# Optimization experiments

Hardware: AMD Instinct MI355X
Metric: run time of the kernel (lower is better)

The kernel has to match this reference:

```python
import jax, jax.numpy as jnp
import numpy as np

NUM_E = 20000   # entities
NUM_R = 200     # relations (rel table has 2*NUM_R rows)
H = 200         # h_dim
TD = 48         # t_dim (UnionTimeEncode: two halves of 24)
HD = TD // 2
L_HIST = 32     # padded per-(batch,k) history list length
HIS_K = 3
N_HIST = 3      # len(his_list_g)
N_LAYERS = 2    # RGCN layers (config.num_layers)
E = 200000      # edges per historical graph
BATCH = 512


def setup_inputs() -> dict:
    key = jax.random.key(0)
    ks = jax.random.split(key, 32)
    nrm = lambda k, shape, s=0.05: (jax.random.normal(k, shape, jnp.float32) * s)
    inp = {}
    # graph / index inputs (int)
    inp['src'] = jax.random.randint(ks[0], (N_HIST, E), 0, NUM_E, jnp.int32)
    inp['dst'] = jax.random.randint(ks[1], (N_HIST, E), 0, NUM_E, jnp.int32)
    inp['etype'] = jax.random.randint(ks[2], (N_HIST, E), 0, 2 * NUM_R, jnp.int32)
    inp['data'] = jax.random.randint(ks[3], (BATCH, 4), 0, NUM_R, jnp.int32)  # s,r,o,t
    inp['his_idx'] = jax.random.randint(ks[4], (BATCH, HIS_K, L_HIST), 0, NUM_E, jnp.int32)
    inp['his_len'] = jax.random.randint(ks[5], (BATCH, HIS_K), 0, L_HIST + 1, jnp.int32)
    # parameters (float)
    inp['ent'] = nrm(ks[6], (NUM_E, H), 0.5)          # EntEmb.ent (normal init)
    inp['loop_weight'] = nrm(ks[7], (H, H))           # EntEmb self-loop weight
    inp['rel'] = nrm(ks[8], (2 * NUM_R, H), 0.5)
    # UnionTimeEncode params (AbsTimeEncode v=0 + CosTimeEncode)
    basis = (1.0 / 10 ** np.linspace(0.0, 9.0, HD)).astype(np.float32)
    inp['abs_freq'] = jnp.asarray(basis)
    inp['abs_phase'] = jnp.zeros((HD,), jnp.float32)
    inp['cos_freq'] = jnp.asarray(basis)
    inp['cos_phase'] = jnp.zeros((HD,), jnp.float32)
    # RGCN (RE-GCN style Union-RGCN layer: msg=(h_src+rel_e)@Wn, mean agg, self-loop)
    inp['Wn'] = nrm(ks[9], (N_LAYERS, H, H))
    inp['Ws'] = nrm(ks[10], (N_LAYERS, H, H))
    # GRUCell (PyTorch layout)
    inp['W_ih'] = nrm(ks[11], (3 * H, H + TD))
    inp['W_hh'] = nrm(ks[12], (3 * H, H))
    inp['b_ih'] = jnp.zeros((3 * H,), jnp.float32)
    inp['b_hh'] = jnp.zeros((3 * H,), jnp.float32)
    # attention fusion
    inp['Wb_w'] = nrm(ks[13], (H, 3 * H + TD))
    inp['Wb_b'] = jnp.zeros((H,), jnp.float32)
    inp['Wc_w'] = nrm(ks[14], (1, H))
    inp['Wc_b'] = jnp.zeros((1,), jnp.float32)
    # decoder (MLP query @ entity table)
    inp['Wd_w'] = nrm(ks[15], (H, 3 * H))
    inp['Wd_b'] = jnp.zeros((H,), jnp.float32)
    return inp


def _l2n(x, eps=1e-12):
    # F.normalize: x / max(||x||, eps)
    n = jnp.linalg.norm(x, axis=-1, keepdims=True)
    return x / jnp.maximum(n, eps)


def reference(src, dst, etype, data, his_idx, his_len,
              ent, loop_weight, rel, abs_freq, abs_phase, cos_freq, cos_phase,
              Wn, Ws, W_ih, W_hh, b_ih, b_hh, Wb_w, Wb_b, Wc_w, Wc_b, Wd_w, Wd_b):
    def tenc(t):  # t: [N,1] float -> [N,TD]
        a = jnp.tanh((t + 1.0) * abs_freq + abs_phase)   # AbsTimeEncode(act=tanh)
        c = jnp.cos(t * cos_freq + cos_phase)            # CosTimeEncode
        return jnp.concatenate([a, c], axis=1)

    s_i, r_i = data[:, 0], data[:, 1]
    ent_e = ent @ loop_weight                  # EntEmb self-loop (dropout=identity, eval)
    rel_n = _l2n(rel)
    prev = _l2n(ent_e)                         # g_list[0]
    tim_cnt = N_HIST
    ones_e = jnp.ones((E,), jnp.float32)
    for i in range(N_HIST):                    # python loop over fixed #graphs
        si, di, ei = src[i], dst[i], etype[i]
        deg = jax.ops.segment_sum(ones_e, di, num_segments=NUM_E)         # in-degree
        inv = 1.0 / jnp.maximum(deg, 1.0)
        # g.update_all(copy_src, mean): zero in-degree nodes -> 0
        agg = jax.ops.segment_sum(prev[si], di, num_segments=NUM_E) * inv[:, None]
        h = _l2n(jnp.where(deg[:, None] > 0, agg, 0.0))
        tim_cnt -= 1
        tim = jnp.where(deg > 0, float(tim_cnt), 100.0)[:, None]
        te = tenc(tim)                                                     # [NUM_E,TD]
        for l in range(N_LAYERS):              # RGCN
            msg = (h[si] + rel_n[ei]) @ Wn[l]                              # [E,H]
            nagg = jax.ops.segment_sum(msg, di, num_segments=NUM_E) * inv[:, None]
            h = jax.nn.relu(nagg + h @ Ws[l])
        h = _l2n(h)
        # GRUCell(cat([h, te]), prev)
        gi = jnp.concatenate([h, te], axis=1) @ W_ih.T + b_ih
        gh = prev @ W_hh.T + b_hh
        ir, iz, iN = jnp.split(gi, 3, axis=1)
        hr, hz, hN = jnp.split(gh, 3, axis=1)
        rg = jax.nn.sigmoid(ir + hr)
        zg = jax.nn.sigmoid(iz + hz)
        ng = jnp.tanh(iN + rg * hN)
        prev = _l2n((1.0 - zg) * ng + zg * prev)
    out = prev

    q_s, q_r = out[s_i], rel_n[r_i]
    tim_cnt = min(N_HIST, HIS_K)
    s_embs, atts = [], []
    pos = jnp.arange(L_HIST)[None, :]
    for k in range(min(N_HIST, HIS_K)):
        tim_cnt -= 1
        ln = his_len[:, k]
        mask = (pos < ln[:, None]).astype(jnp.float32)                     # [B,L]
        # sparse one-hot mm + divide by length
        tmp = jnp.einsum('blh,bl->bh', out[his_idx[:, k, :]], mask)
        tmp = _l2n(tmp / jnp.maximum(ln, 1).astype(jnp.float32)[:, None])
        tim = jnp.where(ln > 0, float(tim_cnt), 100.0)[:, None]
        te = tenc(tim)                                                     # [B,TD]
        s_embs.append(tmp)
        a = jax.nn.relu(jnp.concatenate([q_s, q_r, tmp, te], 1) @ Wb_w.T + Wb_b)
        atts.append(a @ Wc_w.T + Wc_b)                                     # [B,1]
    att = jax.nn.softmax(jnp.stack(atts, axis=1), axis=1)                  # [B,K,1]
    out2 = jnp.sum(jnp.stack(s_embs, axis=1) * att, axis=1)                # bmm fusion
    # decoder: MLP query scored against all entity states
    q = jax.nn.relu(jnp.concatenate([q_s, q_r, out2], 1) @ Wd_w.T + Wd_b)
    return q @ out.T                                                       # [B,NUM_E]
```

## Files before the change

kernel.cpp:

```cpp
#include <hip/hip_runtime.h>
#include <hip/hip_bf16.h>

#define NUM_E   20000
#define H_DIM   200
#define TD_DIM  48
#define HD_DIM  24
#define L_HIST  32
#define N_HIST  3
#define E_EDGES 200000
#define BATCH   512


__device__ inline float wave_sum64(float x) {
    #pragma unroll
    for (int m = 1; m < 64; m <<= 1) x += __shfl_xor(x, m);
    return x;
}

__device__ inline ushort f2bf(float f) {
    unsigned u = __float_as_uint(f);
    u += 0x7fffu + ((u >> 16) & 1u);
    return (ushort)(u >> 16);
}
__device__ inline float bf2f(ushort u) {
    return __uint_as_float(((unsigned)u) << 16);
}
__device__ inline float4 bf4_to_f4(ushort4 v) {
    return (float4){bf2f(v.x), bf2f(v.y), bf2f(v.z), bf2f(v.w)};
}

__global__ void fill_i32(int* __restrict__ p, long n, int v) {
    long i = (long)blockIdx.x * blockDim.x + threadIdx.x;
    if (i < n) p[i] = v;
}

__global__ void bias_sum(float* __restrict__ bsum, const float* __restrict__ b_ih,
                         const float* __restrict__ b_hh) {
    int j = blockIdx.x * 256 + threadIdx.x;
    if (j < 600) bsum[j] = b_ih[j] + b_hh[j];
}

__global__ void cvt_bf16_k(ushort* __restrict__ o, const float* __restrict__ in, long n) {
    long i = (long)blockIdx.x * 256 + threadIdx.x;
    if (i < n) o[i] = f2bf(in[i]);
}

__global__ void make_lo(ushort* __restrict__ lo, const float* __restrict__ x,
                        const ushort* __restrict__ hi, long n) {
    long i = (long)blockIdx.x * 256 + threadIdx.x;
    if (i < n) lo[i] = f2bf(x[i] - bf2f(hi[i]));
}

__global__ void tcvt_bf16_k(ushort* __restrict__ o, const float* __restrict__ in, int R, int C) {
    int i = blockIdx.x * 256 + threadIdx.x;
    if (i >= R * C) return;
    int r = i / C, c = i - r * C;
    o[(size_t)c * R + r] = f2bf(in[i]);
}

struct Segs {
    const float* A[4];
    const float* B[4];
    int lda[4], ldb[4], Ks[4];
    int nseg, Ktot;
};

__device__ inline void seg_find(const Segs& sg, int gk, int& s, int& loc) {
    s = 0; loc = gk;
    #pragma unroll
    for (int t = 0; t < 3; t++) {
        if (s + 1 < sg.nseg && loc >= sg.Ks[s]) { loc -= sg.Ks[s]; s++; }
    }
}

__global__ __launch_bounds__(256) void sgemm_splitk(
    float* __restrict__ P, const Segs sg, int M, int N, int nbx, int nby,
    int KS, int tpc)
{
    __shared__ float As[32][68];
    __shared__ float Bs[32][68];

    int tot = nbx * nby;
    int tot_all = tot * KS;
    int chunk = (tot_all + 7) >> 3;
    int v = (int)(blockIdx.x & 7) * chunk + (int)(blockIdx.x >> 3);
    if (v >= tot_all) return;
    int kc = v / tot;
    int tile = v - kc * tot;
    int by = tile / nbx, bx = tile - by * nbx;
    const int bn = bx * 64;
    const int bm = by * 64;
    const int tid = threadIdx.x;
    const int m0 = (tid >> 4) * 4;
    const int n0 = (tid & 15) * 4;

    float acc[4][4];
    #pragma unroll
    for (int i = 0; i < 4; i++)
        #pragma unroll
        for (int j = 0; j < 4; j++) acc[i][j] = 0.f;

    const int Ktot = sg.Ktot;
    const int ntile = (Ktot + 31) / 32;
    const int kt0 = kc * tpc;
    const int kt1 = min(ntile, kt0 + tpc);

    const int a_m  = tid & 31;
    const int a_k4 = (tid >> 5) * 4;
    const int b1_n = tid & 63;
    const int b1_k = (tid >> 6) * 4;

    float4 ra[2], rb[2];
    auto loadA = [&](int k0) {
        int gk = k0 + a_k4;
        bool kin = gk < Ktot;
        int s = 0, loc = 0;
        if (kin) seg_find(sg, gk, s, loc);
        const float* Ab = sg.A[s];
        const int lda = sg.lda[s];
        #pragma unroll
        for (int r = 0; r < 2; r++) {
            int row = bm + a_m + 32 * r;
            float4 vv = {0.f, 0.f, 0.f, 0.f};
            if (kin && row < M) vv = *(const float4*)(Ab + (size_t)row * lda + loc);
            ra[r] = vv;
        }
    };
    auto loadB = [&](int k0) {
        #pragma unroll
        for (int r = 0; r < 2; r++) {
            int k4 = b1_k + 16 * r;
            int gk = k0 + k4;
            bool kin = gk < Ktot;
            int s = 0, loc = 0;
            if (kin) seg_find(sg, gk, s, loc);
            const float* Bb = sg.B[s];
            const int ldb = sg.ldb[s];
            int gn = bn + b1_n;
            float4 vv = {0.f, 0.f, 0.f, 0.f};
            if (kin && gn < N) vv = *(const float4*)(Bb + (size_t)gn * ldb + loc);
            rb[r] = vv;
        }
    };

    if (kt0 < kt1) {
        loadA(kt0 * 32); loadB(kt0 * 32);
        for (int t = kt0; t < kt1; t++) {
            #pragma unroll
            for (int r = 0; r < 2; r++) {
                int m = a_m + 32 * r;
                As[a_k4 + 0][m] = ra[r].x;
                As[a_k4 + 1][m] = ra[r].y;
                As[a_k4 + 2][m] = ra[r].z;
                As[a_k4 + 3][m] = ra[r].w;
            }
            #pragma unroll
            for (int r = 0; r < 2; r++) {
                int k4 = b1_k + 16 * r;
                Bs[k4 + 0][b1_n] = rb[r].x;
                Bs[k4 + 1][b1_n] = rb[r].y;
                Bs[k4 + 2][b1_n] = rb[r].z;
                Bs[k4 + 3][b1_n] = rb[r].w;
            }
            __syncthreads();
            if (t + 1 < kt1) { loadA((t + 1) * 32); loadB((t + 1) * 32); }
            #pragma unroll 8
            for (int kk = 0; kk < 32; kk++) {
                float4 b = *(float4*)&Bs[kk][n0];
                float4 av = *(float4*)&As[kk][m0];
                float a[4] = {av.x, av.y, av.z, av.w};
                #pragma unroll
                for (int i = 0; i < 4; i++) {
                    acc[i][0] += a[i] * b.x;
                    acc[i][1] += a[i] * b.y;
                    acc[i][2] += a[i] * b.z;
                    acc[i][3] += a[i] * b.w;
                }
            }
            __syncthreads();
        }
    }

    int col = bn + n0;
    if (col < N) {
        #pragma unroll
        for (int i = 0; i < 4; i++) {
            int row = bm + m0 + i;
            if (row < M) {
                float4 o = {acc[i][0], acc[i][1], acc[i][2], acc[i][3]};
                *(float4*)(P + ((size_t)kc * M + row) * N + col) = o;
            }
        }
    }
}

__global__ void reduce_relu(float* __restrict__ out, const float* __restrict__ P,
                            const float* __restrict__ bias, int MN, int N, int KS)
{
    int i = blockIdx.x * 256 + threadIdx.x;
    if (i >= MN) return;
    float s = bias[i % N];
    for (int k = 0; k < KS; k++) s += P[(size_t)k * MN + i];
    out[i] = fmaxf(s, 0.f);
}

__global__ void reduce_relu_split(ushort* __restrict__ qhi, ushort* __restrict__ qlo,
                                  const float* __restrict__ P, const float* __restrict__ bias,
                                  int MN, int N, int KS)
{
    int i = blockIdx.x * 256 + threadIdx.x;
    if (i >= MN) return;
    float s = bias[i % N];
    for (int k = 0; k < KS; k++) s += P[(size_t)k * MN + i];
    s = fmaxf(s, 0.f);
    ushort h = f2bf(s);
    qhi[i] = h;
    qlo[i] = f2bf(s - bf2f(h));
}

typedef __attribute__((ext_vector_type(8))) short bfrag;
typedef __attribute__((ext_vector_type(4))) float ffrag;

struct BfSegs {
    const ushort* A[3];
    const ushort* B[3];
    int lda[3], ldb[3], Ks[3];
    int nseg, Ktot;
};

__device__ inline void bseg_find(const BfSegs& sg, int gk, int& s, int& loc) {
    s = 0; loc = gk;
    #pragma unroll
    for (int t = 0; t < 2; t++) {
        if (s + 1 < sg.nseg && loc >= sg.Ks[s]) { loc -= sg.Ks[s]; s++; }
    }
}

struct GemmDesc {
    BfSegs sg;
    float* C;
    ushort* Cb;
    const float* bias;
    int M, N, ldc;
    int act, flags, order;
    int nbx, nby, blk0, nblk;
};

struct MultiArgs {
    GemmDesc d[3];
    int nd;
    int tot;
};

template<int DI>
__device__ __forceinline__ void gemm_body(const MultiArgs& ma, int v,
                                          ushort* __restrict__ Als,
                                          ushort* __restrict__ Bls)
{
    const GemmDesc& D = ma.d[DI];
    const BfSegs& sg = D.sg;
    const int tile = v - D.blk0;
    int by, bx;
    if (D.order == 0) { by = tile / D.nbx; bx = tile - by * D.nbx; }
    else              { bx = tile / D.nby; by = tile - bx * D.nby; }
    const int bm = by * 64, bn = bx * 64;
    const int M = D.M, N = D.N;

    const int tid  = threadIdx.x;
    const int lane = tid & 63;
    const int w    = tid >> 6;
    const int wm   = (w & 1) * 2;
    const int wn   = (w >> 1) * 2;

    ffrag acc[2][2];
    #pragma unroll
    for (int i = 0; i < 2; i++)
        #pragma unroll
        for (int j = 0; j < 2; j++) acc[i][j] = (ffrag){0.f, 0.f, 0.f, 0.f};

    const int Ktot = sg.Ktot;
    const int nkt = (Ktot + 63) >> 6;

    int a_m[2], a_kq[2], a_wc[2];
    #pragma unroll
    for (int i = 0; i < 2; i++) {
        int c = i * 256 + tid;
        a_m[i] = c & 63; a_kq[i] = c >> 6;
        a_wc[i] = ((a_m[i] >> 4) * 2 + (a_kq[i] >> 2)) * 64 + (a_kq[i] & 3) * 16 + (a_m[i] & 15);
    }
    int b_n[2], b_kq[2], b_wc[2];
    #pragma unroll
    for (int i = 0; i < 2; i++) {
        int c = i * 256 + tid;
        b_n[i] = c & 63; b_kq[i] = c >> 6;
        b_wc[i] = ((b_n[i] >> 4) * 2 + (b_kq[i] >> 2)) * 64 + (b_kq[i] & 3) * 16 + (b_n[i] & 15);
    }

    uint4 ra[2], rb[2];
    auto loadA = [&](int k0) {
        #pragma unroll
        for (int i = 0; i < 2; i++) {
            int gk = k0 + a_kq[i] * 8;
            int row = bm + a_m[i];
            uint4 vv = {0u, 0u, 0u, 0u};
            if (gk < Ktot && row < M) {
                int s, loc; bseg_find(sg, gk, s, loc);
                vv = *(const uint4*)(sg.A[s] + (size_t)row * sg.lda[s] + loc);
            }
            ra[i] = vv;
        }
    };
    auto loadB = [&](int k0) {
        #pragma unroll
        for (int i = 0; i < 2; i++) {
            int gk = k0 + b_kq[i] * 8;
            int gn = bn + b_n[i];
            uint4 vv = {0u, 0u, 0u, 0u};
            if (gk < Ktot && gn < N) {
                int s, loc; bseg_find(sg, gk, s, loc);
                vv = *(const uint4*)(sg.B[s] + (size_t)gn * sg.ldb[s] + loc);
            }
            rb[i] = vv;
        }
    };

    loadA(0); loadB(0);

    for (int t = 0; t < nkt; t++) {
        #pragma unroll
        for (int i = 0; i < 2; i++) *(uint4*)(&Als[a_wc[i] * 8]) = ra[i];
        #pragma unroll
        for (int i = 0; i < 2; i++) *(uint4*)(&Bls[b_wc[i] * 8]) = rb[i];
        __syncthreads();

        if (t + 1 < nkt) { loadA((t + 1) << 6); loadB((t + 1) << 6); }

        #pragma unroll
        for (int kt = 0; kt < 2; kt++) {
            bfrag af[2], bf[2];
            #pragma unroll
            for (int i = 0; i < 2; i++)
                af[i] = *(const bfrag*)(&Als[(((wm + i) * 2 + kt) * 64 + lane) * 8]);
            #pragma unroll
            for (int j = 0; j < 2; j++)
                bf[j] = *(const bfrag*)(&Bls[(((wn + j) * 2 + kt) * 64 + lane) * 8]);
            #pragma unroll
            for (int i = 0; i < 2; i++)
                #pragma unroll
                for (int j = 0; j < 2; j++)
                    acc[i][j] = __builtin_amdgcn_mfma_f32_16x16x32_bf16(af[i], bf[j], acc[i][j], 0, 0, 0);
        }
        __syncthreads();
    }

    const int rbase = (lane >> 4) * 4;
    const int cl = lane & 15;
    #pragma unroll
    for (int j = 0; j < 2; j++) {
        int col = bn + (wn + j) * 16 + cl;
        if (col >= N) continue;
        float bv = D.bias ? D.bias[col] : 0.f;
        #pragma unroll
        for (int i = 0; i < 2; i++) {
            int mrow = bm + (wm + i) * 16 + rbase;
            #pragma unroll
            for (int r = 0; r < 4; r++) {
                int row = mrow + r;
                if (row < M) {
                    float o = acc[i][j][r] + bv;
                    if (D.act == 1) o = fmaxf(o, 0.f);
                    else if (D.act == 2) o = 1.f / (1.f + expf(-o));
                    if (D.flags & 1) D.C[(size_t)row * D.ldc + col] = o;
                    if (D.flags & 2) D.Cb[(size_t)row * D.ldc + col] = f2bf(o);
                }
            }
        }
    }
}

__global__ __launch_bounds__(256) void mfma_multi(MultiArgs ma)
{
    __shared__ __align__(16) ushort Als[4096];
    __shared__ __align__(16) ushort Bls[4096];

    int tot = ma.tot;
    int chunk = (tot + 7) >> 3;
    int v = (int)(blockIdx.x & 7) * chunk + (int)(blockIdx.x >> 3);
    if (v >= tot) return;

    int di = 0;
    if (ma.nd > 1 && v >= ma.d[1].blk0) di = 1;
    if (ma.nd > 2 && v >= ma.d[2].blk0) di = 2;

    if (di == 0)      gemm_body<0>(ma, v, Als, Bls);
    else if (di == 1) gemm_body<1>(ma, v, Als, Bls);
    else              gemm_body<2>(ma, v, Als, Bls);
}


__global__ void count_dst(const int* __restrict__ di, int* __restrict__ cnt, int E) {
    int e = blockIdx.x * 256 + threadIdx.x;
    if (e < E) atomicAdd(&cnt[di[e]], 1);
}

__global__ __launch_bounds__(1024) void scan_rows(
    const int* __restrict__ cnt, int* __restrict__ row_start, int* __restrict__ cursor,
    float* __restrict__ degf, float* __restrict__ invd)
{
    __shared__ int part[1024];
    const int CH = (NUM_E + 1023) / 1024;
    int t = threadIdx.x;
    int base = t * CH;
    int local[32];
    int s = 0;
    for (int j = 0; j < CH; j++) {
        int idx = base + j;
        int c = (idx < NUM_E) ? cnt[idx] : 0;
        local[j] = s; s += c;
    }
    part[t] = s;
    __syncthreads();
    for (int off = 1; off < 1024; off <<= 1) {
        int vv = (t >= off) ? part[t - off] : 0;
        __syncthreads();
        part[t] += vv;
        __syncthreads();
    }
    int pre = (t == 0) ? 0 : part[t - 1];
    for (int j = 0; j < CH; j++) {
        int idx = base + j;
        if (idx < NUM_E) {
            int rs = pre + local[j];
            row_start[idx] = rs;
            cursor[idx] = rs;
            int c = cnt[idx];
            degf[idx] = (float)c;
            invd[idx] = 1.f / fmaxf((float)c, 1.f);
        }
    }
    if (t == 1023) row_start[NUM_E] = part[1023];
}

__global__ void build_perm(const int* __restrict__ si, const int* __restrict__ di,
                           const int* __restrict__ ei, int* __restrict__ cursor,
                           int* __restrict__ ssrc, int* __restrict__ setype, int E)
{
    int e = blockIdx.x * 256 + threadIdx.x;
    if (e >= E) return;
    int pos = atomicAdd(&cursor[di[e]], 1);
    ssrc[pos]   = si[e];
    setype[pos] = ei[e];
}


__global__ __launch_bounds__(256) void seg_gather_norm_bf(
    ushort* __restrict__ bh, const ushort* __restrict__ bprev,
    const int* __restrict__ ssrc, const int* __restrict__ row_start,
    const float* __restrict__ invd)
{
    int v = blockIdx.x * 4 + (threadIdx.x >> 6);
    int lane = threadIdx.x & 63;
    if (v >= NUM_E) return;
    int s0 = row_start[v], s1 = row_start[v + 1];
    bool act = lane < 50;
    float4 acc = {0.f, 0.f, 0.f, 0.f};
    int j = s0;
    for (; j + 1 < s1; j += 2) {
        int sa = ssrc[j], sb = ssrc[j + 1];
        if (act) {
            float4 xa = bf4_to_f4(*(const ushort4*)(bprev + (long)sa * H_DIM + lane * 4));
            float4 xb = bf4_to_f4(*(const ushort4*)(bprev + (long)sb * H_DIM + lane * 4));
            acc.x += xa.x + xb.x; acc.y += xa.y + xb.y;
            acc.z += xa.z + xb.z; acc.w += xa.w + xb.w;
        }
    }
    if (j < s1) {
        int sa = ssrc[j];
        if (act) {
            float4 xa = bf4_to_f4(*(const ushort4*)(bprev + (long)sa * H_DIM + lane * 4));
            acc.x += xa.x; acc.y += xa.y; acc.z += xa.z; acc.w += xa.w;
        }
    }
    float iv = invd[v];
    acc.x *= iv; acc.y *= iv; acc.z *= iv; acc.w *= iv;
    float ss = act ? (acc.x*acc.x + acc.y*acc.y + acc.z*acc.z + acc.w*acc.w) : 0.f;
    ss = wave_sum64(ss);
    float r = 1.f / fmaxf(sqrtf(ss), 1e-12f);
    if (act) {
        ushort4 ob = {f2bf(acc.x * r), f2bf(acc.y * r), f2bf(acc.z * r), f2bf(acc.w * r)};
        *(ushort4*)(bh + (long)v * H_DIM + lane * 4) = ob;
    }
}

__global__ __launch_bounds__(256) void seg_gather_layer_bf(
    ushort* __restrict__ btmp, const ushort* __restrict__ bh, const ushort* __restrict__ brel,
    const int* __restrict__ ssrc, const int* __restrict__ setype,
    const int* __restrict__ row_start, const float* __restrict__ invd)
{
    int v = blockIdx.x * 4 + (threadIdx.x >> 6);
    int lane = threadIdx.x & 63;
    if (v >= NUM_E) return;
    int s0 = row_start[v], s1 = row_start[v + 1];
    bool act = lane < 50;
    float4 acc = {0.f, 0.f, 0.f, 0.f};
    for (int j = s0; j < s1; j++) {
        int s = ssrc[j];
        int t = setype[j];
        if (act) {
            float4 x = bf4_to_f4(*(const ushort4*)(bh   + (long)s * H_DIM + lane * 4));
            float4 y = bf4_to_f4(*(const ushort4*)(brel + (long)t * H_DIM + lane * 4));
            acc.x += x.x + y.x; acc.y += x.y + y.y;
            acc.z += x.z + y.z; acc.w += x.w + y.w;
        }
    }
    float iv = invd[v];
    if (act) {
        ushort4 ob = {f2bf(acc.x * iv), f2bf(acc.y * iv), f2bf(acc.z * iv), f2bf(acc.w * iv)};
        *(ushort4*)(btmp + (long)v * H_DIM + lane * 4) = ob;
    }
}


__global__ __launch_bounds__(256) void l2norm_rows4(
    float* __restrict__ out, ushort* __restrict__ bout,
    const float* __restrict__ in, int nrows)
{
    int v = blockIdx.x * 4 + (threadIdx.x >> 6);
    int lane = threadIdx.x & 63;
    if (v >= nrows) return;
    bool act = lane < 50;
    float4 x = {0.f, 0.f, 0.f, 0.f};
    if (act) x = *(const float4*)(in + (long)v * H_DIM + lane * 4);
    float ss = x.x*x.x + x.y*x.y + x.z*x.z + x.w*x.w;
    ss = wave_sum64(ss);
    float r = 1.f / fmaxf(sqrtf(ss), 1e-12f);
    if (act) {
        long base = (long)v * H_DIM + lane * 4;
        float4 o = {x.x * r, x.y * r, x.z * r, x.w * r};
        *(float4*)(out + base) = o;
        if (bout) {
            ushort4 ob = {f2bf(o.x), f2bf(o.y), f2bf(o.z), f2bf(o.w)};
            *(ushort4*)(bout + base) = ob;
        }
    }
}

__global__ __launch_bounds__(256) void l2norm_bf4(ushort* __restrict__ b, int nrows)
{
    int v = blockIdx.x * 4 + (threadIdx.x >> 6);
    int lane = threadIdx.x & 63;
    if (v >= nrows) return;
    bool act = lane < 50;
    float4 x = {0.f, 0.f, 0.f, 0.f};
    long base = (long)v * H_DIM + lane * 4;
    if (act) x = bf4_to_f4(*(const ushort4*)(b + base));
    float ss = x.x*x.x + x.y*x.y + x.z*x.z + x.w*x.w;
    ss = wave_sum64(ss);
    float r = 1.f / fmaxf(sqrtf(ss), 1e-12f);
    if (act) {
        ushort4 ob = {f2bf(x.x * r), f2bf(x.y * r), f2bf(x.z * r), f2bf(x.w * r)};
        *(ushort4*)(b + base) = ob;
    }
}

__global__ void tenc_ent(ushort* __restrict__ bte, const float* __restrict__ deg,
                         const float* __restrict__ af, const float* __restrict__ ap,
                         const float* __restrict__ cf, const float* __restrict__ cp,
                         float tcnt, int M)
{
    int idx = blockIdx.x * 256 + threadIdx.x;
    if (idx >= M * TD_DIM) return;
    int v = idx / TD_DIM, j = idx % TD_DIM;
    float t = (deg[v] > 0.f) ? tcnt : 100.0f;
    float val;
    if (j < HD_DIM) val = tanhf((t + 1.f) * af[j] + ap[j]);
    else            val = cosf(t * cf[j - HD_DIM] + cp[j - HD_DIM]);
    bte[idx] = f2bf(val);
}

__global__ __launch_bounds__(256) void gru_fused(
    float* __restrict__ prev, ushort* __restrict__ bprev, const float* __restrict__ rz,
    const float* __restrict__ iN, const float* __restrict__ hN)
{
    int v = blockIdx.x * 4 + (threadIdx.x >> 6);
    int lane = threadIdx.x & 63;
    if (v >= NUM_E) return;
    bool act = lane < 50;
    long b200 = (long)v * H_DIM + lane * 4;
    long b400 = (long)v * 400 + lane * 4;
    float4 o = {0.f, 0.f, 0.f, 0.f};
    if (act) {
        float4 r4 = *(const float4*)(rz + b400);
        float4 z4 = *(const float4*)(rz + b400 + 200);
        float4 n4 = *(const float4*)(iN + b200);
        float4 g4 = *(const float4*)(hN + b200);
        float4 p4 = *(const float4*)(prev + b200);
        float ngx = tanhf(n4.x + r4.x * g4.x);
        float ngy = tanhf(n4.y + r4.y * g4.y);
        float ngz = tanhf(n4.z + r4.z * g4.z);
        float ngw = tanhf(n4.w + r4.w * g4.w);
        o.x = (1.f - z4.x) * ngx + z4.x * p4.x;
        o.y = (1.f - z4.y) * ngy + z4.y * p4.y;
        o.z = (1.f - z4.z) * ngz + z4.z * p4.z;
        o.w = (1.f - z4.w) * ngw + z4.w * p4.w;
    }
    float ss = o.x*o.x + o.y*o.y + o.z*o.z + o.w*o.w;
    ss = wave_sum64(ss);
    float r = 1.f / fmaxf(sqrtf(ss), 1e-12f);
    if (act) {
        float4 wv = {o.x * r, o.y * r, o.z * r, o.w * r};
        *(float4*)(prev + b200) = wv;
        ushort4 ob = {f2bf(wv.x), f2bf(wv.y), f2bf(wv.z), f2bf(wv.w)};
        *(ushort4*)(bprev + b200) = ob;
    }
}


__global__ void gather_qs_qr3(float* __restrict__ qs3, float* __restrict__ qr3,
                              const float* __restrict__ out, const float* __restrict__ reln,
                              const int* __restrict__ data)
{
    long i = (long)blockIdx.x * 256 + threadIdx.x;
    if (i >= (long)BATCH * H_DIM) return;
    int b = (int)(i / H_DIM), j = (int)(i % H_DIM);
    float vs = out[(long)data[b * 4 + 0] * H_DIM + j];
    float vr = reln[(long)data[b * 4 + 1] * H_DIM + j];
    const long S = (long)BATCH * H_DIM;
    qs3[i] = vs; qs3[i + S] = vs; qs3[i + 2*S] = vs;
    qr3[i] = vr; qr3[i + S] = vr; qr3[i + 2*S] = vr;
}

__global__ __launch_bounds__(64) void semb_kernel(
    float* __restrict__ semb, const float* __restrict__ out,
    const int* __restrict__ his_idx, const int* __restrict__ his_len)
{
    int b = blockIdx.x, k = blockIdx.y;
    int lane = threadIdx.x;
    int ln = his_len[b * 3 + k];
    if (ln > L_HIST) ln = L_HIST;
    float vals[4] = {0.f, 0.f, 0.f, 0.f};
    for (int l = 0; l < ln; l++) {
        int idx = his_idx[((long)b * 3 + k) * L_HIST + l];
        #pragma unroll
        for (int t = 0; t < 4; t++) {
            int j = lane + t * 64;
            if (j < H_DIM) vals[t] += out[(long)idx * H_DIM + j];
        }
    }
    float scale = 1.f / fmaxf((float)ln, 1.f);
    float ss = 0.f;
    #pragma unroll
    for (int t = 0; t < 4; t++) { vals[t] *= scale; ss += vals[t] * vals[t]; }
    ss = wave_sum64(ss);
    float r = 1.f / fmaxf(sqrtf(ss), 1e-12f);
    #pragma unroll
    for (int t = 0; t < 4; t++) {
        int j = lane + t * 64;
        if (j < H_DIM) semb[((long)k * BATCH + b) * H_DIM + j] = vals[t] * r;
    }
}

__global__ void tenc_batch(float* __restrict__ teb, const int* __restrict__ his_len,
                           const float* __restrict__ af, const float* __restrict__ ap,
                           const float* __restrict__ cf, const float* __restrict__ cp)
{
    int idx = blockIdx.x * 256 + threadIdx.x;
    if (idx >= 3 * BATCH * TD_DIM) return;
    int k = idx / (BATCH * TD_DIM);
    int rem = idx - k * (BATCH * TD_DIM);
    int b = rem / TD_DIM, j = rem % TD_DIM;
    int ln = his_len[b * 3 + k];
    float t = (ln > 0) ? (float)(2 - k) : 100.0f;
    float val;
    if (j < HD_DIM) val = tanhf((t + 1.f) * af[j] + ap[j]);
    else            val = cosf(t * cf[j - HD_DIM] + cp[j - HD_DIM]);
    teb[idx] = val;
}

__global__ __launch_bounds__(256) void att_logits_rows(
    float* __restrict__ atts, const float* __restrict__ a,
    const float* __restrict__ Wc_w, const float* __restrict__ Wc_b)
{
    int row = blockIdx.x * 4 + (threadIdx.x >> 6);
    int lane = threadIdx.x & 63;
    if (row >= 3 * BATCH) return;
    int k = row >> 9;
    int b = row & 511;
    float s = 0.f;
    for (int j = lane; j < H_DIM; j += 64) s += a[(long)row * H_DIM + j] * Wc_w[j];
    s = wave_sum64(s);
    if (lane == 0) atts[b * 3 + k] = s + Wc_b[0];
}

__global__ void softmax_out2(float* __restrict__ out2, const float* __restrict__ atts,
                             const float* __restrict__ semb)
{
    long i = (long)blockIdx.x * 256 + threadIdx.x;
    if (i >= (long)BATCH * H_DIM) return;
    int b = (int)(i / H_DIM), j = (int)(i % H_DIM);
    float l0 = atts[b * 3 + 0], l1 = atts[b * 3 + 1], l2 = atts[b * 3 + 2];
    float m = fmaxf(l0, fmaxf(l1, l2));
    float e0 = expf(l0 - m), e1 = expf(l1 - m), e2 = expf(l2 - m);
    float s = e0 + e1 + e2;
    float v = (e0 * semb[((long)0 * BATCH + b) * H_DIM + j] +
               e1 * semb[((long)1 * BATCH + b) * H_DIM + j] +
               e2 * semb[((long)2 * BATCH + b) * H_DIM + j]) / s;
    out2[i] = v;
}


extern "C" void kernel_launch(void* const* d_in, const int* in_sizes, int n_in,
                              void* d_out, int out_size, void* d_ws, size_t ws_size,
                              hipStream_t stream)
{
    (void)in_sizes; (void)n_in; (void)out_size; (void)ws_size;

    const int*   src     = (const int*)d_in[0];
    const int*   dst     = (const int*)d_in[1];
    const int*   etype   = (const int*)d_in[2];
    const int*   data    = (const int*)d_in[3];
    const int*   his_idx = (const int*)d_in[4];
    const int*   his_len = (const int*)d_in[5];
    const float* ent     = (const float*)d_in[6];
    const float* loop_w  = (const float*)d_in[7];
    const float* rel     = (const float*)d_in[8];
    const float* af      = (const float*)d_in[9];
    const float* ap      = (const float*)d_in[10];
    const float* cf      = (const float*)d_in[11];
    const float* cp      = (const float*)d_in[12];
    const float* Wn      = (const float*)d_in[13];
    const float* Ws      = (const float*)d_in[14];
    const float* W_ih    = (const float*)d_in[15];
    const float* W_hh    = (const float*)d_in[16];
    const float* b_ih    = (const float*)d_in[17];
    const float* b_hh    = (const float*)d_in[18];
    const float* Wb_w    = (const float*)d_in[19];
    const float* Wb_b    = (const float*)d_in[20];
    const float* Wc_w    = (const float*)d_in[21];
    const float* Wc_b    = (const float*)d_in[22];
    const float* Wd_w    = (const float*)d_in[23];
    const float* Wd_b    = (const float*)d_in[24];
    float* out_p = (float*)d_out;

    float* wp = (float*)d_ws;
    size_t off = 0;
    auto alloc = [&](size_t n) {
        size_t n4 = (n + 3) & ~(size_t)3;
        float* p = wp + off; off += n4; return p;
    };
    const long nE200 = (long)NUM_E * H_DIM;
    float* prev   = alloc(nE200);
    float* h1     = alloc(nE200);
    float* tmp    = alloc(nE200);
    float* rz     = out_p;
    ushort* bh0   = (ushort*)alloc(nE200 / 2);
    ushort* bh1   = (ushort*)alloc(nE200 / 2);
    ushort* btmp  = (ushort*)alloc(nE200 / 2);
    ushort* bprev = (ushort*)alloc(nE200 / 2);
    ushort* plo   = (ushort*)alloc(nE200 / 2);
    ushort* bte   = (ushort*)alloc((size_t)NUM_E * TD_DIM / 2);
    ushort* brel  = (ushort*)alloc(400 * H_DIM / 2);
    ushort* bW_ih = (ushort*)alloc(600 * 248 / 2);
    ushort* bW_hh = (ushort*)alloc(600 * 200 / 2);
    ushort* bWn_t = (ushort*)alloc(2 * 200 * 200 / 2);
    ushort* bWs_t = (ushort*)alloc(2 * 200 * 200 / 2);
    ushort* bLp_t = (ushort*)alloc(200 * 200 / 2);
    ushort* qhi   = (ushort*)alloc(BATCH * H_DIM / 2);
    ushort* qlo   = (ushort*)alloc(BATCH * H_DIM / 2);
    float* degf   = alloc(NUM_E);
    float* invd   = alloc(NUM_E);
    float* reln   = alloc(400 * H_DIM);
    float* bsum   = alloc(1024);
    float* qs3    = alloc(3 * BATCH * H_DIM);
    float* qr3    = alloc(3 * BATCH * H_DIM);
    float* semb   = alloc(3 * BATCH * H_DIM);
    float* teb    = alloc(3 * BATCH * TD_DIM);
    float* abuf   = alloc(3 * BATCH * H_DIM);
    float* atts   = alloc(2048);
    float* out2   = alloc(BATCH * H_DIM);
    int* cnt       = (int*)alloc(NUM_E);
    int* row_start = (int*)alloc(NUM_E + 4);
    int* cursor    = (int*)alloc(NUM_E);
    int* ssrc      = (int*)alloc(E_EDGES);
    int* setype    = (int*)alloc(E_EDGES);

    auto nblk = [](long n) { return (unsigned)((n + 255) / 256); };

    auto bseg1 = [](const ushort* A, int la, const ushort* B, int lb, int K) {
        BfSegs s{}; s.A[0]=A; s.lda[0]=la; s.B[0]=B; s.ldb[0]=lb; s.Ks[0]=K;
        s.nseg=1; s.Ktot=K; return s;
    };
    auto bseg2 = [](const ushort* A0, int la0, const ushort* B0, int lb0, int K0,
                    const ushort* A1, int la1, const ushort* B1, int lb1, int K1) {
        BfSegs s{}; s.A[0]=A0; s.lda[0]=la0; s.B[0]=B0; s.ldb[0]=lb0; s.Ks[0]=K0;
        s.A[1]=A1; s.lda[1]=la1; s.B[1]=B1; s.ldb[1]=lb1; s.Ks[1]=K1;
        s.nseg=2; s.Ktot=K0+K1; return s;
    };
    auto bseg3 = [](const ushort* A0, int la0, const ushort* B0, int lb0, int K0,
                    const ushort* A1, int la1, const ushort* B1, int lb1, int K1,
                    const ushort* A2, int la2, const ushort* B2, int lb2, int K2) {
        BfSegs s{}; s.A[0]=A0; s.lda[0]=la0; s.B[0]=B0; s.ldb[0]=lb0; s.Ks[0]=K0;
        s.A[1]=A1; s.lda[1]=la1; s.B[1]=B1; s.ldb[1]=lb1; s.Ks[1]=K1;
        s.A[2]=A2; s.lda[2]=la2; s.B[2]=B2; s.ldb[2]=lb2; s.Ks[2]=K2;
        s.nseg=3; s.Ktot=K0+K1+K2; return s;
    };

    auto desc = [](const BfSegs& sg, float* C, ushort* Cb, const float* bias,
                   int M, int N, int ldc, int act, int flags, int order) {
        GemmDesc D{}; D.sg=sg; D.C=C; D.Cb=Cb; D.bias=bias;
        D.M=M; D.N=N; D.ldc=ldc; D.act=act; D.flags=flags; D.order=order;
        D.nbx=(N+63)>>6; D.nby=(M+63)>>6; D.nblk=D.nbx*D.nby; D.blk0=0;
        return D;
    };
    auto launch_multi = [&](GemmDesc* ds, int nd) {
        MultiArgs ma{};
        int tot = 0;
        for (int i = 0; i < nd; i++) { ds[i].blk0 = tot; tot += ds[i].nblk; ma.d[i] = ds[i]; }
        ma.nd = nd; ma.tot = tot;
        unsigned grid = (unsigned)(((tot + 7) >> 3) << 3);
        mfma_multi<<<grid, 256, 0, stream>>>(ma);
    };

    auto seg3 = [](const float* A0, int la0, const float* B0, int lb0, int K0,
                   const float* A1, int la1, const float* B1, int lb1, int K1,
                   const float* A2, int la2, const float* B2, int lb2, int K2) {
        Segs s{}; s.A[0]=A0; s.lda[0]=la0; s.B[0]=B0; s.ldb[0]=lb0; s.Ks[0]=K0;
        s.A[1]=A1; s.lda[1]=la1; s.B[1]=B1; s.ldb[1]=lb1; s.Ks[1]=K1;
        s.A[2]=A2; s.lda[2]=la2; s.B[2]=B2; s.ldb[2]=lb2; s.Ks[2]=K2;
        s.nseg=3; s.Ktot=K0+K1+K2; return s;
    };
    auto seg4 = [](const float* A0, int la0, const float* B0, int lb0, int K0,
                   const float* A1, int la1, const float* B1, int lb1, int K1,
                   const float* A2, int la2, const float* B2, int lb2, int K2,
                   const float* A3, int la3, const float* B3, int lb3, int K3) {
        Segs s{}; s.A[0]=A0; s.lda[0]=la0; s.B[0]=B0; s.ldb[0]=lb0; s.Ks[0]=K0;
        s.A[1]=A1; s.lda[1]=la1; s.B[1]=B1; s.ldb[1]=lb1; s.Ks[1]=K1;
        s.A[2]=A2; s.lda[2]=la2; s.B[2]=B2; s.ldb[2]=lb2; s.Ks[2]=K2;
        s.A[3]=A3; s.lda[3]=la3; s.B[3]=B3; s.ldb[3]=lb3; s.Ks[3]=K3;
        s.nseg=4; s.Ktot=K0+K1+K2+K3; return s;
    };
    auto splitk = [&](float* P, const Segs& sg, int M, int N, int KS) {
        int nbx = (N + 63) >> 6;
        int nby = (M + 63) >> 6;
        int ntile = (sg.Ktot + 31) / 32;
        int tpc = (ntile + KS - 1) / KS;
        int tot_all = nbx * nby * KS;
        unsigned grid = (unsigned)(((tot_all + 7) >> 3) << 3);
        sgemm_splitk<<<grid, 256, 0, stream>>>(P, sg, M, N, nbx, nby, KS, tpc);
    };

    const unsigned r4 = (NUM_E + 3) / 4;

    l2norm_rows4<<<100, 256, 0, stream>>>(reln, brel, rel, 400);
    bias_sum<<<3, 256, 0, stream>>>(bsum, b_ih, b_hh);
    cvt_bf16_k<<<nblk(600L*248), 256, 0, stream>>>(bW_ih, W_ih, 600L*248);
    cvt_bf16_k<<<nblk(600L*200), 256, 0, stream>>>(bW_hh, W_hh, 600L*200);
    tcvt_bf16_k<<<nblk(40000), 256, 0, stream>>>(bLp_t, loop_w, 200, 200);
    tcvt_bf16_k<<<nblk(40000), 256, 0, stream>>>(bWn_t,          Wn,          200, 200);
    tcvt_bf16_k<<<nblk(40000), 256, 0, stream>>>(bWn_t + 40000,  Wn + 40000,  200, 200);
    tcvt_bf16_k<<<nblk(40000), 256, 0, stream>>>(bWs_t,          Ws,          200, 200);
    tcvt_bf16_k<<<nblk(40000), 256, 0, stream>>>(bWs_t + 40000,  Ws + 40000,  200, 200);

    cvt_bf16_k<<<nblk(nE200), 256, 0, stream>>>(btmp, ent, nE200);
    {
        GemmDesc d0 = desc(bseg1(btmp, H_DIM, bLp_t, H_DIM, H_DIM),
                           tmp, nullptr, nullptr, NUM_E, H_DIM, H_DIM, 0, 1, 0);
        launch_multi(&d0, 1);
    }
    l2norm_rows4<<<r4, 256, 0, stream>>>(prev, bprev, tmp, NUM_E);

    for (int i = 0; i < N_HIST; i++) {
        const int* si = src   + (long)i * E_EDGES;
        const int* di = dst   + (long)i * E_EDGES;
        const int* ei = etype + (long)i * E_EDGES;
        float tcnt = (float)(N_HIST - 1 - i);

        fill_i32<<<nblk(NUM_E), 256, 0, stream>>>(cnt, NUM_E, 0);
        count_dst<<<nblk(E_EDGES), 256, 0, stream>>>(di, cnt, E_EDGES);
        scan_rows<<<1, 1024, 0, stream>>>(cnt, row_start, cursor, degf, invd);
        build_perm<<<nblk(E_EDGES), 256, 0, stream>>>(si, di, ei, cursor, ssrc, setype, E_EDGES);

        seg_gather_norm_bf<<<r4, 256, 0, stream>>>(bh0, bprev, ssrc, row_start, invd);
        tenc_ent<<<nblk((long)NUM_E * TD_DIM), 256, 0, stream>>>(bte, degf, af, ap, cf, cp, tcnt, NUM_E);

        seg_gather_layer_bf<<<r4, 256, 0, stream>>>(btmp, bh0, brel, ssrc, setype, row_start, invd);
        {
            GemmDesc d0 = desc(bseg2(btmp, H_DIM, bWn_t,         H_DIM, H_DIM,
                                     bh0,  H_DIM, bWs_t,         H_DIM, H_DIM),
                               nullptr, bh1, nullptr, NUM_E, H_DIM, H_DIM, 1, 2, 0);
            launch_multi(&d0, 1);
        }
        seg_gather_layer_bf<<<r4, 256, 0, stream>>>(btmp, bh1, brel, ssrc, setype, row_start, invd);
        {
            GemmDesc d0 = desc(bseg2(btmp, H_DIM, bWn_t + 40000, H_DIM, H_DIM,
                                     bh1,  H_DIM, bWs_t + 40000, H_DIM, H_DIM),
                               nullptr, bh0, nullptr, NUM_E, H_DIM, H_DIM, 1, 2, 0);
            launch_multi(&d0, 1);
        }
        l2norm_bf4<<<r4, 256, 0, stream>>>(bh0, NUM_E);

        {
            GemmDesc d3[3];
            d3[0] = desc(bseg3(bh0,   H_DIM,  bW_ih,       248, H_DIM,
                               bte,   TD_DIM, bW_ih + 200, 248, TD_DIM,
                               bprev, H_DIM,  bW_hh,       200, H_DIM),
                         rz, nullptr, bsum, NUM_E, 400, 400, 2, 1, 0);
            d3[1] = desc(bseg2(bh0, H_DIM,  bW_ih + 400*248,       248, H_DIM,
                               bte, TD_DIM, bW_ih + 400*248 + 200, 248, TD_DIM),
                         h1, nullptr, b_ih + 400, NUM_E, H_DIM, H_DIM, 0, 1, 0);
            d3[2] = desc(bseg1(bprev, H_DIM, bW_hh + 400*200, 200, H_DIM),
                         tmp, nullptr, b_hh + 400, NUM_E, H_DIM, H_DIM, 0, 1, 0);
            launch_multi(d3, 3);
        }

        gru_fused<<<r4, 256, 0, stream>>>(prev, bprev, rz, h1, tmp);
    }

    gather_qs_qr3<<<nblk((long)BATCH * H_DIM), 256, 0, stream>>>(qs3, qr3, prev, reln, data);
    semb_kernel<<<dim3(BATCH, 3), 64, 0, stream>>>(semb, prev, his_idx, his_len);
    tenc_batch<<<nblk(3L * BATCH * TD_DIM), 256, 0, stream>>>(teb, his_len, af, ap, cf, cp);

    {
        const int KS = 8;
        const int MN = 3 * BATCH * H_DIM;
        splitk(h1, seg4(qs3, H_DIM,  Wb_w,       648, H_DIM,
                        qr3, H_DIM,  Wb_w + 200, 648, H_DIM,
                        semb, H_DIM, Wb_w + 400, 648, H_DIM,
                        teb, TD_DIM, Wb_w + 600, 648, TD_DIM),
               3 * BATCH, H_DIM, KS);
        reduce_relu<<<nblk(MN), 256, 0, stream>>>(abuf, h1, Wb_b, MN, H_DIM, KS);
    }
    att_logits_rows<<<(3 * BATCH + 3) / 4, 256, 0, stream>>>(atts, abuf, Wc_w, Wc_b);
    softmax_out2<<<nblk((long)BATCH * H_DIM), 256, 0, stream>>>(out2, atts, semb);

    {
        const int KS = 8;
        const int MN = BATCH * H_DIM;
        splitk(tmp, seg3(qs3, H_DIM,  Wd_w,       600, H_DIM,
                         qr3, H_DIM,  Wd_w + 200, 600, H_DIM,
                         out2, H_DIM, Wd_w + 400, 600, H_DIM),
               BATCH, H_DIM, KS);
        reduce_relu_split<<<nblk(MN), 256, 0, stream>>>(qhi, qlo, tmp, Wd_b, MN, H_DIM, KS);
    }

    make_lo<<<nblk(nE200), 256, 0, stream>>>(plo, prev, bprev, nE200);

    {
        GemmDesc d0 = desc(bseg3(qhi, H_DIM, bprev, H_DIM, H_DIM,
                                 qhi, H_DIM, plo,   H_DIM, H_DIM,
                                 qlo, H_DIM, bprev, H_DIM, H_DIM),
                           out_p, nullptr, nullptr, BATCH, NUM_E, NUM_E, 0, 1, 1);
        launch_multi(&d0, 1);
    }
}
```

Before: 1.297 ms.

## Enlarge GEMM M-tile to 128, unroll edge gather by two, tabulate time encoding

The shared MFMA GEMM kernel now computes 128x64 tiles instead of 64x64, with each wave holding four M fragments. This doubles A-tile LDS and register use but reuses B loads across more rows and halves the block count. The per-destination edge gather in the RGCN layer is unrolled by two so more independent loads are in flight. The per-entity time encoding is precomputed into a two-row table and copied with vector stores, replacing per-element tanh/cos evaluation.

```diff
diff --git a/kernel.cpp b/kernel.cpp
--- a/kernel.cpp
+++ b/kernel.cpp
@@ -263,29 +263,29 @@
     int by, bx;
     if (D.order == 0) { by = tile / D.nbx; bx = tile - by * D.nbx; }
     else              { bx = tile / D.nby; by = tile - bx * D.nby; }
-    const int bm = by * 64, bn = bx * 64;
+    const int bm = by * 128, bn = bx * 64;
     const int M = D.M, N = D.N;
 
     const int tid  = threadIdx.x;
     const int lane = tid & 63;
     const int w    = tid >> 6;
-    const int wm   = (w & 1) * 2;
+    const int wm   = (w & 1) * 4;
     const int wn   = (w >> 1) * 2;
 
-    ffrag acc[2][2];
+    ffrag acc[4][2];
     #pragma unroll
-    for (int i = 0; i < 2; i++)
+    for (int i = 0; i < 4; i++)
         #pragma unroll
         for (int j = 0; j < 2; j++) acc[i][j] = (ffrag){0.f, 0.f, 0.f, 0.f};
 
     const int Ktot = sg.Ktot;
     const int nkt = (Ktot + 63) >> 6;
 
-    int a_m[2], a_kq[2], a_wc[2];
+    int a_m[4], a_kq[4], a_wc[4];
     #pragma unroll
-    for (int i = 0; i < 2; i++) {
+    for (int i = 0; i < 4; i++) {
         int c = i * 256 + tid;
-        a_m[i] = c & 63; a_kq[i] = c >> 6;
+        a_m[i] = c & 127; a_kq[i] = c >> 7;
         a_wc[i] = ((a_m[i] >> 4) * 2 + (a_kq[i] >> 2)) * 64 + (a_kq[i] & 3) * 16 + (a_m[i] & 15);
     }
     int b_n[2], b_kq[2], b_wc[2];
@@ -296,10 +296,10 @@
         b_wc[i] = ((b_n[i] >> 4) * 2 + (b_kq[i] >> 2)) * 64 + (b_kq[i] & 3) * 16 + (b_n[i] & 15);
     }
 
-    uint4 ra[2], rb[2];
+    uint4 ra[4], rb[2];
     auto loadA = [&](int k0) {
         #pragma unroll
-        for (int i = 0; i < 2; i++) {
+        for (int i = 0; i < 4; i++) {
             int gk = k0 + a_kq[i] * 8;
             int row = bm + a_m[i];
             uint4 vv = {0u, 0u, 0u, 0u};
@@ -328,7 +328,7 @@
 
     for (int t = 0; t < nkt; t++) {
         #pragma unroll
-        for (int i = 0; i < 2; i++) *(uint4*)(&Als[a_wc[i] * 8]) = ra[i];
+        for (int i = 0; i < 4; i++) *(uint4*)(&Als[a_wc[i] * 8]) = ra[i];
         #pragma unroll
         for (int i = 0; i < 2; i++) *(uint4*)(&Bls[b_wc[i] * 8]) = rb[i];
         __syncthreads();
@@ -337,15 +337,15 @@
 
         #pragma unroll
         for (int kt = 0; kt < 2; kt++) {
-            bfrag af[2], bf[2];
+            bfrag af[4], bf[2];
             #pragma unroll
-            for (int i = 0; i < 2; i++)
+            for (int i = 0; i < 4; i++)
                 af[i] = *(const bfrag*)(&Als[(((wm + i) * 2 + kt) * 64 + lane) * 8]);
             #pragma unroll
             for (int j = 0; j < 2; j++)
                 bf[j] = *(const bfrag*)(&Bls[(((wn + j) * 2 + kt) * 64 + lane) * 8]);
             #pragma unroll
-            for (int i = 0; i < 2; i++)
+            for (int i = 0; i < 4; i++)
                 #pragma unroll
                 for (int j = 0; j < 2; j++)
                     acc[i][j] = __builtin_amdgcn_mfma_f32_16x16x32_bf16(af[i], bf[j], acc[i][j], 0, 0, 0);
@@ -361,7 +361,7 @@
         if (col >= N) continue;
         float bv = D.bias ? D.bias[col] : 0.f;
         #pragma unroll
-        for (int i = 0; i < 2; i++) {
+        for (int i = 0; i < 4; i++) {
             int mrow = bm + (wm + i) * 16 + rbase;
             #pragma unroll
             for (int r = 0; r < 4; r++) {
@@ -380,7 +380,7 @@
 
 __global__ __launch_bounds__(256) void mfma_multi(MultiArgs ma)
 {
-    __shared__ __align__(16) ushort Als[4096];
+    __shared__ __align__(16) ushort Als[8192];
     __shared__ __align__(16) ushort Bls[4096];
 
     int tot = ma.tot;
@@ -503,7 +503,22 @@
     int s0 = row_start[v], s1 = row_start[v + 1];
     bool act = lane < 50;
     float4 acc = {0.f, 0.f, 0.f, 0.f};
-    for (int j = s0; j < s1; j++) {
+    int j = s0;
+    for (; j + 1 < s1; j += 2) {
+        int sa = ssrc[j], ta = setype[j];
+        int sb = ssrc[j + 1], tb = setype[j + 1];
+        if (act) {
+            float4 xa = bf4_to_f4(*(const ushort4*)(bh   + (long)sa * H_DIM + lane * 4));
+            float4 ya = bf4_to_f4(*(const ushort4*)(brel + (long)ta * H_DIM + lane * 4));
+            float4 xb = bf4_to_f4(*(const ushort4*)(bh   + (long)sb * H_DIM + lane * 4));
+            float4 yb = bf4_to_f4(*(const ushort4*)(brel + (long)tb * H_DIM + lane * 4));
+            acc.x += (xa.x + ya.x) + (xb.x + yb.x);
+            acc.y += (xa.y + ya.y) + (xb.y + yb.y);
+            acc.z += (xa.z + ya.z) + (xb.z + yb.z);
+            acc.w += (xa.w + ya.w) + (xb.w + yb.w);
+        }
+    }
+    if (j < s1) {
         int s = ssrc[j];
         int t = setype[j];
         if (act) {
@@ -563,19 +578,30 @@
     }
 }
 
-__global__ void tenc_ent(ushort* __restrict__ bte, const float* __restrict__ deg,
-                         const float* __restrict__ af, const float* __restrict__ ap,
-                         const float* __restrict__ cf, const float* __restrict__ cp,
-                         float tcnt, int M)
+__global__ void tenc_table(ushort* __restrict__ tbl, const float* __restrict__ af,
+                           const float* __restrict__ ap, const float* __restrict__ cf,
+                           const float* __restrict__ cp, float tcnt)
+{
+    int j = threadIdx.x;
+    if (j >= 128) return;
+    int half = j >> 6;
+    int jj = j & 63;
+    if (jj >= TD_DIM) return;
+    float t = half ? 100.0f : tcnt;
+    float val;
+    if (jj < HD_DIM) val = tanhf((t + 1.f) * af[jj] + ap[jj]);
+    else             val = cosf(t * cf[jj - HD_DIM] + cp[jj - HD_DIM]);
+    tbl[half * 64 + jj] = f2bf(val);
+}
+
+__global__ void tenc_fill(ushort* __restrict__ bte, const float* __restrict__ deg,
+                          const ushort* __restrict__ tbl, int M)
 {
     int idx = blockIdx.x * 256 + threadIdx.x;
-    if (idx >= M * TD_DIM) return;
-    int v = idx / TD_DIM, j = idx % TD_DIM;
-    float t = (deg[v] > 0.f) ? tcnt : 100.0f;
-    float val;
-    if (j < HD_DIM) val = tanhf((t + 1.f) * af[j] + ap[j]);
-    else            val = cosf(t * cf[j - HD_DIM] + cp[j - HD_DIM]);
-    bte[idx] = f2bf(val);
+    if (idx >= M * 6) return;
+    int v = idx / 6, c = idx - v * 6;
+    int base = (deg[v] > 0.f) ? 0 : 64;
+    *(uint4*)(bte + (long)v * TD_DIM + c * 8) = *(const uint4*)(tbl + base + c * 8);
 }
 
 __global__ __launch_bounds__(256) void gru_fused(
@@ -767,6 +793,7 @@
     ushort* bLp_t = (ushort*)alloc(200 * 200 / 2);
     ushort* qhi   = (ushort*)alloc(BATCH * H_DIM / 2);
     ushort* qlo   = (ushort*)alloc(BATCH * H_DIM / 2);
+    ushort* ttbl  = (ushort*)alloc(64);
     float* degf   = alloc(NUM_E);
     float* invd   = alloc(NUM_E);
     float* reln   = alloc(400 * H_DIM);
@@ -809,7 +836,7 @@
                    int M, int N, int ldc, int act, int flags, int order) {
         GemmDesc D{}; D.sg=sg; D.C=C; D.Cb=Cb; D.bias=bias;
         D.M=M; D.N=N; D.ldc=ldc; D.act=act; D.flags=flags; D.order=order;
-        D.nbx=(N+63)>>6; D.nby=(M+63)>>6; D.nblk=D.nbx*D.nby; D.blk0=0;
+        D.nbx=(N+63)>>6; D.nby=(M+127)>>7; D.nblk=D.nbx*D.nby; D.blk0=0;
         return D;
     };
     auto launch_multi = [&](GemmDesc* ds, int nd) {
@@ -881,7 +908,8 @@
         build_perm<<<nblk(E_EDGES), 256, 0, stream>>>(si, di, ei, cursor, ssrc, setype, E_EDGES);
 
         seg_gather_norm_bf<<<r4, 256, 0, stream>>>(bh0, bprev, ssrc, row_start, invd);
-        tenc_ent<<<nblk((long)NUM_E * TD_DIM), 256, 0, stream>>>(bte, degf, af, ap, cf, cp, tcnt, NUM_E);
+        tenc_table<<<1, 128, 0, stream>>>(ttbl, af, ap, cf, cp, tcnt);
+        tenc_fill<<<nblk((long)NUM_E * 6), 256, 0, stream>>>(bte, degf, ttbl, NUM_E);
 
         seg_gather_layer_bf<<<r4, 256, 0, stream>>>(btmp, bh0, brel, ssrc, setype, row_start, invd);
         {
```

Measured after the change: 1.343 ms. 1.04x slower.
